# Kernel tuning notes

Measured on AMD Instinct MI355X. Metric: run time of the kernel, lower is better.

The kernel has to match this reference:

```python
import jax, jax.numpy as jnp
import numpy as np

EPS = 1e-8
B, N, K, UNITS, FDIMS = 4, 20000, 8, 64, 64
S = K + 1

def _norm(x):
    # euclidean norm over last axis with safe (zero) gradient at 0, same forward as tf.norm
    s = jnp.sum(x * x, axis=-1, keepdims=True)
    return jnp.where(s == 0, 0.0, jnp.sqrt(jnp.where(s == 0, 1.0, s)))

def _conv1d(x, w, b):
    # x: (B,N,S,Cin), w: (3,Cin,Cout); keras Conv1D(kernel=3, padding='same') over the S (1+K) axis + relu
    Bx, Nx, Sx, C = x.shape
    y = jax.lax.conv_general_dilated(x.reshape(Bx * Nx, Sx, C), w, (1,), 'SAME',
                                     dimension_numbers=('NWC', 'WIO', 'NWC'))
    return jax.nn.relu(y + b).reshape(Bx, Nx, Sx, -1)

def _encode(x, ws, bs):
    # encode() from source: channel-sum residual pre-add, then residual loop
    r = _conv1d(x + jnp.sum(x, -1, keepdims=True), ws[0], bs[0])
    for w, b in zip(ws[1:], bs[1:]):
        r = r + _conv1d(r + jnp.sum(r, -1, keepdims=True), w, b)
    return r

def setup_inputs():
    key = jax.random.key(0)
    ks = jax.random.split(key, 32)
    it = iter(list(ks))
    def w(shape, k):
        fan_in = shape[-2] * (shape[0] if len(shape) == 3 else 1)
        return (jax.random.normal(k, shape, jnp.float32) / np.float32(np.sqrt(fan_in)))
    inp = {
        'pc': jax.random.normal(next(it), (B, N, S, 4), jnp.float32),
        'feats': jax.random.normal(next(it), (B, N, S, FDIMS), jnp.float32),
    }
    for name, cin in (('pos', 2), ('rel', 2), ('nrm', 1), ('ang', 3)):
        inp[name + '_w0'] = w((3, cin, UNITS), next(it)); inp[name + '_b0'] = jnp.zeros((UNITS,), jnp.float32)
        inp[name + '_w1'] = w((3, UNITS, UNITS), next(it)); inp[name + '_b1'] = jnp.zeros((UNITS,), jnp.float32)
        inp[name + '_w2'] = w((3, UNITS, UNITS), next(it)); inp[name + '_b2'] = jnp.zeros((UNITS,), jnp.float32)
    inp['mlp_w'] = w((2 * UNITS, UNITS), next(it)); inp['mlp_b'] = jnp.zeros((UNITS,), jnp.float32)
    return inp

def reference(pc, feats, pos_w0, pos_b0, pos_w1, pos_b1, pos_w2, pos_b2,
              rel_w0, rel_b0, rel_w1, rel_b1, rel_w2, rel_b2,
              nrm_w0, nrm_b0, nrm_w1, nrm_b1, nrm_w2, nrm_b2,
              ang_w0, ang_b0, ang_w1, ang_b1, ang_w2, ang_b2,
              mlp_w, mlp_b):
    current = pc[:, :, :1]                          # (B,N,1,4)
    diff = current[..., :2] - pc[..., :2]           # (B,N,S,2)
    norms = _norm(pc[..., :2])                      # (B,N,S,1)
    diff_norm = _norm(diff)
    current_norm = _norm(current)                   # norm over all 4 channels, as in source
    num = jnp.sum(diff * current[..., 2:4], axis=-1, keepdims=True)
    den = diff_norm * current_norm + EPS
    angles = 1.0 - jnp.abs(num / den)
    rppe = jnp.concatenate([pc, diff, norms, angles], axis=-1)  # (B,N,S,8)
    pos, rel_pos = rppe[..., :2], rppe[..., 2:4]
    nrm_in, ang_in = rppe[..., 4:5], rppe[..., 5:]  # faithful to source slicing
    pos_e = _encode(pos, [pos_w0, pos_w1, pos_w2], [pos_b0, pos_b1, pos_b2])
    rel_e = _encode(rel_pos, [rel_w0, rel_w1, rel_w2], [rel_b0, rel_b1, rel_b2])
    nrm_e = _encode(nrm_in, [nrm_w0, nrm_w1, nrm_w2], [nrm_b0, nrm_b1, nrm_b2])
    ang_e = _encode(ang_in, [ang_w0, ang_w1, ang_w2], [ang_b0, ang_b1, ang_b2])
    _ = (pos_e, rel_e)  # computed in the source graph but not used in the output
    r = jax.nn.relu(jnp.einsum('bnsc,co->bnso', jnp.concatenate([nrm_e, ang_e], -1), mlp_w) + mlp_b)
    return jnp.concatenate([r, feats], axis=-1)     # (B,N,S,UNITS+FDIMS)
```

## Files before the change

kernel.cpp:

```cpp
#include <hip/hip_runtime.h>

typedef _Float16 f16;
typedef f16 half4 __attribute__((ext_vector_type(4)));
typedef f16 half8 __attribute__((ext_vector_type(8)));
typedef float f32x4 __attribute__((ext_vector_type(4)));

#define Pv 80000
#define G 7
#define AST 72
#define NGRP 11429


__global__ void setup_frags(const float* __restrict__ aw1, const float* __restrict__ aw2,
                            const float* __restrict__ nw1, const float* __restrict__ nw2,
                            const float* __restrict__ mlp_w, f16* __restrict__ ws)
{
  int tid = blockIdx.x*blockDim.x + threadIdx.x;
  if (tid < 7168){
    int L    = tid / 1792;
    int rem  = tid % 1792;
    int q    = (rem % 448) / 64;
    int lane = rem % 64;
    int nt   = rem / 448;
    const float* W = (L==0)?aw1:(L==1)?aw2:(L==2)?nw1:nw2;
    int n = nt*16 + (lane & 15);
    f16 o8[8];
    #pragma unroll
    for (int j=0;j<8;j++){
      int k = q*32 + (lane>>4)*8 + j;
      float v = 0.f;
      if (k < 192) v = W[k*64 + n];
      else if (k < 195){ int tap = k-192; float s=0.f;
        for (int c=0;c<64;c++) s += W[(tap*64+c)*64 + n]; v = s; }
      o8[j] = (f16)v;
    }
    *(half8*)(ws + (size_t)tid*8) = *(half8*)o8;
  } else if (tid < 8192){
    int t2 = tid - 7168;
    int lane = t2 % 64;
    int q    = (t2 / 64) % 4;
    int nt   = t2 / 256;
    int n = nt*16 + (lane & 15);
    f16 o8[8];
    #pragma unroll
    for (int j=0;j<8;j++){
      int k = q*32 + (lane>>4)*8 + j;
      o8[j] = (f16)mlp_w[k*64 + n];
    }
    *(half8*)(ws + 57344 + (size_t)t2*8) = *(half8*)o8;
  }
}

template<int CIN, int CH0>
__device__ __forceinline__ void layer0(f16* A,
    const float* __restrict__ w0, const float* __restrict__ b0, int lane)
{
  float w[3*CIN];
  #pragma unroll
  for (int i=0;i<3*CIN;i++) w[i] = w0[i*64 + lane];
  float bias = b0[lane];
  #pragma unroll 1
  for (int p=0;p<G;p++){
    float x[11][4];
    #pragma unroll
    for (int i=0;i<11;i++){
      half4 h = *(const half4*)(A + (p*11+i)*AST + 68);
      #pragma unroll
      for (int c=0;c<4;c++) x[i][c] = (float)h[c];
    }
    float vals[9];
    #pragma unroll
    for (int s=0;s<9;s++){
      float a = bias;
      #pragma unroll
      for (int t=0;t<3;t++){
        if (CIN == 1){
          a += (2.f * x[s+t][CH0]) * w[t];
        } else {
          float ysum = x[s+t][CH0] + x[s+t][CH0+1] + x[s+t][CH0+2];
          #pragma unroll
          for (int c=0;c<CIN;c++) a += (x[s+t][CH0+c] + ysum) * w[t*CIN+c];
        }
      }
      vals[s] = fmaxf(a, 0.f);
    }
    float rs[9];
    #pragma unroll
    for (int s=0;s<9;s++) rs[s] = vals[s];
    #pragma unroll
    for (int m=1;m<64;m<<=1){
      #pragma unroll
      for (int s=0;s<9;s++) rs[s] += __shfl_xor(rs[s], m);
    }
    #pragma unroll
    for (int s=0;s<9;s++) A[(p*11+1+s)*AST + lane] = (f16)vals[s];
    if (lane == 0){
      #pragma unroll
      for (int s=0;s<9;s++) A[(p*11+1+s)*AST + 64] = (f16)rs[s];
    }
  }
}

template<bool WRITE_RS, bool CARRY_IN, bool CARRY_OUT>
__device__ __forceinline__ void conv_layer(const f16* __restrict__ frag,
    const float* __restrict__ bias, f16* A, int lane, half4 (&cres)[4][4])
{
  const int lo = lane & 15, qd = lane >> 4;
  float bn[4];
  #pragma unroll
  for (int nt=0;nt<4;nt++) bn[nt] = bias[nt*16 + lo];
  f32x4 acc[4][4];
  #pragma unroll
  for (int t=0;t<4;t++)
    #pragma unroll
    for (int nt=0;nt<4;nt++) acc[t][nt] = (f32x4){bn[nt],bn[nt],bn[nt],bn[nt]};

  int abase[4], rbase[4];
  #pragma unroll
  for (int t=0;t<4;t++){
    int m = t*16 + lo; if (m > 62) m = 62;
    int p = m/9, s = m - 9*p;
    abase[t] = ((p*11 + s)*AST)*2 + qd*16;
    rbase[t] = (p*11 + s)*AST + 64;
  }
  #pragma unroll
  for (int q=0;q<7;q++){
    half8 bv[4];
    #pragma unroll
    for (int nt=0;nt<4;nt++)
      bv[nt] = *(const half8*)(frag + ((nt*7 + q)*64 + lane)*8);
    #pragma unroll
    for (int t=0;t<4;t++){
      half8 av;
      if (q < 6){
        av = *(const half8*)((const char*)A + abase[t] + (q>>1)*(AST*2) + (q&1)*64);
      } else {
        const f16* rp = A + rbase[t];
        av = (half8){rp[0], rp[AST], rp[2*AST], (f16)0, (f16)0, (f16)0, (f16)0, (f16)0};
      }
      #pragma unroll
      for (int nt=0;nt<4;nt++)
        acc[t][nt] = __builtin_amdgcn_mfma_f32_16x16x32_f16(av, bv[nt], acc[t][nt], 0, 0, 0);
    }
  }
  #pragma unroll
  for (int t=0;t<4;t++){
    #pragma unroll
    for (int r=0;r<4;r++){
      int mr = t*16 + qd*4 + r;
      int mc = mr > 62 ? 62 : mr;
      int pr = mc/9, sr = mc - 9*pr;
      bool vld = (mr < 63);
      f16* rowA = A + (pr*11 + 1 + sr)*AST;
      float tmp = 0.f, rnew[4];
      #pragma unroll
      for (int nt=0;nt<4;nt++){
        float rold = CARRY_IN ? (float)cres[t][nt][r] : (float)rowA[nt*16 + lo];
        float v = fmaxf(acc[t][nt][r], 0.f) + rold;
        rnew[nt] = v; tmp += v;
        if (CARRY_OUT) cres[t][nt][r] = (f16)v;
      }
      if (WRITE_RS){
        tmp += __shfl_xor(tmp, 1); tmp += __shfl_xor(tmp, 2);
        tmp += __shfl_xor(tmp, 4); tmp += __shfl_xor(tmp, 8);
      }
      if (vld){
        #pragma unroll
        for (int nt=0;nt<4;nt++) rowA[nt*16 + lo] = (f16)rnew[nt];
        if (WRITE_RS && lo == 0) rowA[64] = (f16)tmp;
      }
    }
  }
}

__device__ __forceinline__ void mlp_out(const f16* __restrict__ frag,
    const float* __restrict__ mb, const f16* __restrict__ An, const f16* __restrict__ Aa,
    int lane, int wid, long pbase, float* __restrict__ out)
{
  const int lo = lane & 15, qd = lane >> 4;
  float bn[4];
  #pragma unroll
  for (int nt=0;nt<4;nt++) bn[nt] = mb[nt*16 + lo];
  f32x4 acc[2][4];
  #pragma unroll
  for (int tt=0;tt<2;tt++)
    #pragma unroll
    for (int nt=0;nt<4;nt++) acc[tt][nt] = (f32x4){bn[nt],bn[nt],bn[nt],bn[nt]};

  int aA[2];
  #pragma unroll
  for (int tt=0;tt<2;tt++){
    int m = (wid*2+tt)*16 + lo; if (m > 62) m = 62;
    int p = m/9, s = m - 9*p;
    aA[tt] = ((p*11 + 1 + s)*AST)*2 + qd*16;
  }
  #pragma unroll
  for (int q=0;q<4;q++){
    half8 bv[4];
    #pragma unroll
    for (int nt=0;nt<4;nt++)
      bv[nt] = *(const half8*)(frag + ((nt*4 + q)*64 + lane)*8);
    #pragma unroll
    for (int tt=0;tt<2;tt++){
      half8 av = (q < 2)
        ? *(const half8*)((const char*)An + aA[tt] + q*64)
        : *(const half8*)((const char*)Aa + aA[tt] + (q-2)*64);
      #pragma unroll
      for (int nt=0;nt<4;nt++)
        acc[tt][nt] = __builtin_amdgcn_mfma_f32_16x16x32_f16(av, bv[nt], acc[tt][nt], 0, 0, 0);
    }
  }
  #pragma unroll
  for (int tt=0;tt<2;tt++){
    #pragma unroll
    for (int r=0;r<4;r++){
      int mr = (wid*2+tt)*16 + qd*4 + r;
      int mc = mr > 62 ? 62 : mr;
      int pr = mc/9, sr = mc - 9*pr;
      long pg = pbase + pr;
      if (mr < 63 && pg < Pv){
        float* op = out + ((long)(pg*9 + sr))*128 + lo;
        #pragma unroll
        for (int nt=0;nt<4;nt++) op[nt*16] = fmaxf(acc[tt][nt][r], 0.f);
      }
    }
  }
}

__global__ __launch_bounds__(128, 2) void locse_main(
    const float* __restrict__ pc, const float* __restrict__ feats,
    const float* __restrict__ nw0, const float* __restrict__ nb0,
    const float* __restrict__ nb1, const float* __restrict__ nb2,
    const float* __restrict__ aw0, const float* __restrict__ ab0,
    const float* __restrict__ ab1, const float* __restrict__ ab2,
    const float* __restrict__ mb,  const f16* __restrict__ frag,
    float* __restrict__ out)
{
  __shared__ __align__(16) f16 A2[2][G*11*AST];
  const int tid  = threadIdx.x;
  const int wid  = tid >> 6, lane = tid & 63;
  const long pbase = (long)blockIdx.x * G;
  f16* Aw = A2[wid];

  {
    const half8 z8 = {(f16)0,(f16)0,(f16)0,(f16)0,(f16)0,(f16)0,(f16)0,(f16)0};
    for (int i = lane; i < G*11*AST/8; i += 64) ((half8*)Aw)[i] = z8;
  }
  if (lane < 63){
    int p = lane/9, s = lane - 9*p;
    long pg = pbase + p;
    if (pg < Pv){
      const float4 v  = *(const float4*)(pc + (pg*9 + s)*4);
      const float4 cu = *(const float4*)(pc + (pg*9)*4);
      float d0 = cu.x - v.x, d1 = cu.y - v.y;
      float n2  = v.x*v.x + v.y*v.y;                        float nrm = n2  > 0.f ? sqrtf(n2)  : 0.f;
      float dn2 = d0*d0 + d1*d1;                            float dn  = dn2 > 0.f ? sqrtf(dn2) : 0.f;
      float cn2 = cu.x*cu.x + cu.y*cu.y + cu.z*cu.z + cu.w*cu.w;
      float cn  = cn2 > 0.f ? sqrtf(cn2) : 0.f;
      float ang = 1.f - fabsf((d0*cu.z + d1*cu.w) / (dn*cn + 1e-8f));
      f16* ip = Aw + (p*11 + 1 + s)*AST + 68;
      ip[0]=(f16)d0; ip[1]=(f16)d1; ip[2]=(f16)nrm; ip[3]=(f16)ang;
    }
  }
  half4 cres[4][4];
  if (wid == 0){
    layer0<3,1>(Aw, aw0, ab0, lane);
    conv_layer<true ,false,true >(frag + 0*14336, ab1, Aw, lane, cres);
    conv_layer<false,true ,false>(frag + 1*14336, ab2, Aw, lane, cres);
  } else {
    layer0<1,0>(Aw, nw0, nb0, lane);
    conv_layer<true ,false,true >(frag + 2*14336, nb1, Aw, lane, cres);
    conv_layer<false,true ,false>(frag + 3*14336, nb2, Aw, lane, cres);
  }
  __syncthreads();
  mlp_out(frag + 57344, mb, A2[1], A2[0], lane, wid, pbase, out);

  {
    const float4* ff = (const float4*)feats + pbase*144;
    float4* op = (float4*)out;
    #pragma unroll 1
    for (int i=0;i<8;i++){
      int idx = i*128 + tid;
      if (idx < G*9*16){
        int ps = idx >> 4, c4 = idx & 15;
        long pg = pbase + ps/9;
        if (pg < Pv)
          op[(pbase*9 + (long)ps)*32 + 16 + c4] = ff[(long)ps*16 + c4];
      }
    }
  }
}

extern "C" void kernel_launch(void* const* d_in, const int* in_sizes, int n_in,
                              void* d_out, int out_size, void* d_ws, size_t ws_size,
                              hipStream_t stream)
{
  const float* pc    = (const float*)d_in[0];
  const float* feats = (const float*)d_in[1];
  const float* nw0=(const float*)d_in[14]; const float* nb0=(const float*)d_in[15];
  const float* nw1=(const float*)d_in[16]; const float* nb1=(const float*)d_in[17];
  const float* nw2=(const float*)d_in[18]; const float* nb2=(const float*)d_in[19];
  const float* aw0=(const float*)d_in[20]; const float* ab0=(const float*)d_in[21];
  const float* aw1=(const float*)d_in[22]; const float* ab1=(const float*)d_in[23];
  const float* aw2=(const float*)d_in[24]; const float* ab2=(const float*)d_in[25];
  const float* mw =(const float*)d_in[26]; const float* mb =(const float*)d_in[27];
  f16* ws  = (f16*)d_ws;
  float* out = (float*)d_out;

  setup_frags<<<32, 256, 0, stream>>>(aw1, aw2, nw1, nw2, mw, ws);
  locse_main<<<NGRP, 128, 0, stream>>>(pc, feats, nw0, nb0, nb1, nb2,
                                       aw0, ab0, ab1, ab2, mb, ws, out);
}
```

Measured before the change: 790.0 us.

## Compute first conv layer with MFMA and compact shared-memory row layout

Replaces the scalar per-lane first-layer convolution, with its 64-lane shuffle reductions, by a single MFMA pass using precomputed fp16 weight fragments that fold in the channel-sum pre-add. The first-layer output is kept in registers as the residual carry. Shared rows per point drop from 11 to 10 by sharing padding rows between neighbouring points, which shrinks LDS. Launch bounds are raised to 4 blocks per CU. The gain depends on register pressure staying low enough for the higher occupancy target, and the first layer now runs in fp16 precision.

```diff
diff --git a/kernel.cpp b/kernel.cpp
--- a/kernel.cpp
+++ b/kernel.cpp
@@ -8,10 +8,12 @@
 #define Pv 80000
 #define G 7
 #define AST 72
+#define NROW (G*10+1)
 #define NGRP 11429
 
 
-__global__ void setup_frags(const float* __restrict__ aw1, const float* __restrict__ aw2,
+__global__ void setup_frags(const float* __restrict__ aw0, const float* __restrict__ nw0,
+                            const float* __restrict__ aw1, const float* __restrict__ aw2,
                             const float* __restrict__ nw1, const float* __restrict__ nw2,
                             const float* __restrict__ mlp_w, f16* __restrict__ ws)
 {
@@ -48,61 +50,33 @@
       o8[j] = (f16)mlp_w[k*64 + n];
     }
     *(half8*)(ws + 57344 + (size_t)t2*8) = *(half8*)o8;
-  }
-}
-
-template<int CIN, int CH0>
-__device__ __forceinline__ void layer0(f16* A,
-    const float* __restrict__ w0, const float* __restrict__ b0, int lane)
-{
-  float w[3*CIN];
-  #pragma unroll
-  for (int i=0;i<3*CIN;i++) w[i] = w0[i*64 + lane];
-  float bias = b0[lane];
-  #pragma unroll 1
-  for (int p=0;p<G;p++){
-    float x[11][4];
-    #pragma unroll
-    for (int i=0;i<11;i++){
-      half4 h = *(const half4*)(A + (p*11+i)*AST + 68);
-      #pragma unroll
-      for (int c=0;c<4;c++) x[i][c] = (float)h[c];
-    }
-    float vals[9];
-    #pragma unroll
-    for (int s=0;s<9;s++){
-      float a = bias;
-      #pragma unroll
-      for (int t=0;t<3;t++){
-        if (CIN == 1){
-          a += (2.f * x[s+t][CH0]) * w[t];
-        } else {
-          float ysum = x[s+t][CH0] + x[s+t][CH0+1] + x[s+t][CH0+2];
-          #pragma unroll
-          for (int c=0;c<CIN;c++) a += (x[s+t][CH0+c] + ysum) * w[t*CIN+c];
-        }
-      }
-      vals[s] = fmaxf(a, 0.f);
-    }
-    float rs[9];
-    #pragma unroll
-    for (int s=0;s<9;s++) rs[s] = vals[s];
-    #pragma unroll
-    for (int m=1;m<64;m<<=1){
-      #pragma unroll
-      for (int s=0;s<9;s++) rs[s] += __shfl_xor(rs[s], m);
-    }
-    #pragma unroll
-    for (int s=0;s<9;s++) A[(p*11+1+s)*AST + lane] = (f16)vals[s];
-    if (lane == 0){
-      #pragma unroll
-      for (int s=0;s<9;s++) A[(p*11+1+s)*AST + 64] = (f16)rs[s];
-    }
-  }
-}
-
-template<bool WRITE_RS, bool CARRY_IN, bool CARRY_OUT>
-__device__ __forceinline__ void conv_layer(const f16* __restrict__ frag,
+  } else if (tid < 8704){
+    int t3   = tid - 8192;
+    int lane = t3 & 63;
+    int nt   = (t3 >> 6) & 3;
+    bool isang = t3 < 256;
+    int n  = nt*16 + (lane & 15);
+    int qd = lane >> 4;
+    f16 o8[8];
+    #pragma unroll
+    for (int j=0;j<8;j++){
+      int k = qd*8 + j;
+      float v = 0.f;
+      if (isang){
+        if (k < 9){ int tap = k/3, c = k%3;
+          float s3 = aw0[(tap*3+0)*64+n] + aw0[(tap*3+1)*64+n] + aw0[(tap*3+2)*64+n];
+          v = aw0[(tap*3+c)*64+n] + s3; }
+      } else {
+        if (k < 3) v = 2.f * nw0[k*64+n];
+      }
+      o8[j] = (f16)v;
+    }
+    *(half8*)(ws + (isang ? 65536 : 67584) + ((size_t)(nt*64+lane))*8) = *(half8*)o8;
+  }
+}
+
+template<bool IS_ANG>
+__device__ __forceinline__ void layer0_mfma(const f16* __restrict__ frag,
     const float* __restrict__ bias, f16* A, int lane, half4 (&cres)[4][4])
 {
   const int lo = lane & 15, qd = lane >> 4;
@@ -115,13 +89,77 @@
     #pragma unroll
     for (int nt=0;nt<4;nt++) acc[t][nt] = (f32x4){bn[nt],bn[nt],bn[nt],bn[nt]};
 
-  int abase[4], rbase[4];
+  half8 bv[4];
+  #pragma unroll
+  for (int nt=0;nt<4;nt++) bv[nt] = *(const half8*)(frag + ((nt*64+lane))*8);
+
+  const f16 Z = (f16)0;
   #pragma unroll
   for (int t=0;t<4;t++){
     int m = t*16 + lo; if (m > 62) m = 62;
     int p = m/9, s = m - 9*p;
-    abase[t] = ((p*11 + s)*AST)*2 + qd*16;
-    rbase[t] = (p*11 + s)*AST + 64;
+    const f16* ibp = A + (p*10 + s)*AST + 68;
+    half4 h0 = *(const half4*)(ibp);
+    half4 h1 = *(const half4*)(ibp + AST);
+    half4 h2 = *(const half4*)(ibp + 2*AST);
+    half8 av = (half8){Z,Z,Z,Z,Z,Z,Z,Z};
+    if (IS_ANG){
+      if (qd == 0)      av = (half8){h0[1],h0[2],h0[3],h1[1],h1[2],h1[3],h2[1],h2[2]};
+      else if (qd == 1) av = (half8){h2[3],Z,Z,Z,Z,Z,Z,Z};
+    } else {
+      if (qd == 0)      av = (half8){h0[0],h1[0],h2[0],Z,Z,Z,Z,Z};
+    }
+    #pragma unroll
+    for (int nt=0;nt<4;nt++)
+      acc[t][nt] = __builtin_amdgcn_mfma_f32_16x16x32_f16(av, bv[nt], acc[t][nt], 0, 0, 0);
+  }
+  #pragma unroll
+  for (int t=0;t<4;t++){
+    #pragma unroll
+    for (int r=0;r<4;r++){
+      int mr = t*16 + qd*4 + r;
+      int mc = mr > 62 ? 62 : mr;
+      int pr = mc/9, sr = mc - 9*pr;
+      bool vld = (mr < 63);
+      f16* rowA = A + (pr*10 + 1 + sr)*AST;
+      float tmp = 0.f;
+      #pragma unroll
+      for (int nt=0;nt<4;nt++){
+        float v = fmaxf(acc[t][nt][r], 0.f);
+        cres[t][nt][r] = (f16)v; tmp += v;
+      }
+      tmp += __shfl_xor(tmp, 1); tmp += __shfl_xor(tmp, 2);
+      tmp += __shfl_xor(tmp, 4); tmp += __shfl_xor(tmp, 8);
+      if (vld){
+        #pragma unroll
+        for (int nt=0;nt<4;nt++) rowA[nt*16 + lo] = cres[t][nt][r];
+        if (lo == 0) rowA[64] = (f16)tmp;
+      }
+    }
+  }
+}
+
+template<bool WRITE_RS, bool CARRY_OUT>
+__device__ __forceinline__ void conv_layer(const f16* __restrict__ frag,
+    const float* __restrict__ bias, f16* A, int lane, half4 (&cres)[4][4])
+{
+  const int lo = lane & 15, qd = lane >> 4;
+  float bn[4];
+  #pragma unroll
+  for (int nt=0;nt<4;nt++) bn[nt] = bias[nt*16 + lo];
+  f32x4 acc[4][4];
+  #pragma unroll
+  for (int t=0;t<4;t++)
+    #pragma unroll
+    for (int nt=0;nt<4;nt++) acc[t][nt] = (f32x4){bn[nt],bn[nt],bn[nt],bn[nt]};
+
+  int abase[4], rbase[4];
+  #pragma unroll
+  for (int t=0;t<4;t++){
+    int m = t*16 + lo; if (m > 62) m = 62;
+    int p = m/9, s = m - 9*p;
+    abase[t] = ((p*10 + s)*AST)*2 + qd*16;
+    rbase[t] = (p*10 + s)*AST + 64;
   }
   #pragma unroll
   for (int q=0;q<7;q++){
@@ -151,11 +189,11 @@
       int mc = mr > 62 ? 62 : mr;
       int pr = mc/9, sr = mc - 9*pr;
       bool vld = (mr < 63);
-      f16* rowA = A + (pr*11 + 1 + sr)*AST;
+      f16* rowA = A + (pr*10 + 1 + sr)*AST;
       float tmp = 0.f, rnew[4];
       #pragma unroll
       for (int nt=0;nt<4;nt++){
-        float rold = CARRY_IN ? (float)cres[t][nt][r] : (float)rowA[nt*16 + lo];
+        float rold = (float)cres[t][nt][r];
         float v = fmaxf(acc[t][nt][r], 0.f) + rold;
         rnew[nt] = v; tmp += v;
         if (CARRY_OUT) cres[t][nt][r] = (f16)v;
@@ -192,7 +230,7 @@
   for (int tt=0;tt<2;tt++){
     int m = (wid*2+tt)*16 + lo; if (m > 62) m = 62;
     int p = m/9, s = m - 9*p;
-    aA[tt] = ((p*11 + 1 + s)*AST)*2 + qd*16;
+    aA[tt] = ((p*10 + 1 + s)*AST)*2 + qd*16;
   }
   #pragma unroll
   for (int q=0;q<4;q++){
@@ -227,16 +265,15 @@
   }
 }
 
-__global__ __launch_bounds__(128, 2) void locse_main(
+__global__ __launch_bounds__(128, 4) void locse_main(
     const float* __restrict__ pc, const float* __restrict__ feats,
-    const float* __restrict__ nw0, const float* __restrict__ nb0,
-    const float* __restrict__ nb1, const float* __restrict__ nb2,
-    const float* __restrict__ aw0, const float* __restrict__ ab0,
+    const float* __restrict__ nb0, const float* __restrict__ nb1,
+    const float* __restrict__ nb2, const float* __restrict__ ab0,
     const float* __restrict__ ab1, const float* __restrict__ ab2,
     const float* __restrict__ mb,  const f16* __restrict__ frag,
     float* __restrict__ out)
 {
-  __shared__ __align__(16) f16 A2[2][G*11*AST];
+  __shared__ __align__(16) f16 A2[2][NROW*AST];
   const int tid  = threadIdx.x;
   const int wid  = tid >> 6, lane = tid & 63;
   const long pbase = (long)blockIdx.x * G;
@@ -244,7 +281,7 @@
 
   {
     const half8 z8 = {(f16)0,(f16)0,(f16)0,(f16)0,(f16)0,(f16)0,(f16)0,(f16)0};
-    for (int i = lane; i < G*11*AST/8; i += 64) ((half8*)Aw)[i] = z8;
+    for (int i = lane; i < NROW*AST/8; i += 64) ((half8*)Aw)[i] = z8;
   }
   if (lane < 63){
     int p = lane/9, s = lane - 9*p;
@@ -258,19 +295,19 @@
       float cn2 = cu.x*cu.x + cu.y*cu.y + cu.z*cu.z + cu.w*cu.w;
       float cn  = cn2 > 0.f ? sqrtf(cn2) : 0.f;
       float ang = 1.f - fabsf((d0*cu.z + d1*cu.w) / (dn*cn + 1e-8f));
-      f16* ip = Aw + (p*11 + 1 + s)*AST + 68;
+      f16* ip = Aw + (p*10 + 1 + s)*AST + 68;
       ip[0]=(f16)d0; ip[1]=(f16)d1; ip[2]=(f16)nrm; ip[3]=(f16)ang;
     }
   }
   half4 cres[4][4];
   if (wid == 0){
-    layer0<3,1>(Aw, aw0, ab0, lane);
-    conv_layer<true ,false,true >(frag + 0*14336, ab1, Aw, lane, cres);
-    conv_layer<false,true ,false>(frag + 1*14336, ab2, Aw, lane, cres);
+    layer0_mfma<true >(frag + 65536, ab0, Aw, lane, cres);
+    conv_layer<true ,true >(frag + 0*14336, ab1, Aw, lane, cres);
+    conv_layer<false,false>(frag + 1*14336, ab2, Aw, lane, cres);
   } else {
-    layer0<1,0>(Aw, nw0, nb0, lane);
-    conv_layer<true ,false,true >(frag + 2*14336, nb1, Aw, lane, cres);
-    conv_layer<false,true ,false>(frag + 3*14336, nb2, Aw, lane, cres);
+    layer0_mfma<false>(frag + 67584, nb0, Aw, lane, cres);
+    conv_layer<true ,true >(frag + 2*14336, nb1, Aw, lane, cres);
+    conv_layer<false,false>(frag + 3*14336, nb2, Aw, lane, cres);
   }
   __syncthreads();
   mlp_out(frag + 57344, mb, A2[1], A2[0], lane, wid, pbase, out);
@@ -307,7 +344,7 @@
   f16* ws  = (f16*)d_ws;
   float* out = (float*)d_out;
 
-  setup_frags<<<32, 256, 0, stream>>>(aw1, aw2, nw1, nw2, mw, ws);
-  locse_main<<<NGRP, 128, 0, stream>>>(pc, feats, nw0, nb0, nb1, nb2,
-                                       aw0, ab0, ab1, ab2, mb, ws, out);
-}
+  setup_frags<<<34, 256, 0, stream>>>(aw0, nw0, aw1, aw2, nw1, nw2, mw, ws);
+  locse_main<<<NGRP, 128, 0, stream>>>(pc, feats, nb0, nb1, nb2,
+                                       ab0, ab1, ab2, mb, ws, out);
+}
```

Result: slower. 1.128 ms (+42.8%).
